# Performance work log

Hardware: AMD Instinct MI355X
Metric: run time of the kernel (lower is better)

## Reference

```python
import jax, jax.numpy as jnp
import numpy as np

T, D, H = 2048, 1024, 16
HS = D // H  # head_size = 64
DFF = 4 * D
LN_EPS = 1e-6


def layernorm(x, scale, bias, eps=LN_EPS):
    mu = jnp.mean(x, axis=-1, keepdims=True)
    var = jnp.mean(jnp.square(x - mu), axis=-1, keepdims=True)
    return (x - mu) * jax.lax.rsqrt(var + eps) * scale + bias


def setup_inputs() -> dict:
    key = jax.random.key(0)
    ks = jax.random.split(key, 12)
    s_in = 1.0 / np.sqrt(D)
    s_ff = 1.0 / np.sqrt(DFF)
    return {
        "x": jax.random.normal(ks[0], (T, D), jnp.float32),
        "Wq": jax.random.normal(ks[1], (H, D, HS), jnp.float32) * s_in,
        "Wk": jax.random.normal(ks[2], (H, D, HS), jnp.float32) * s_in,
        "Wv": jax.random.normal(ks[3], (H, D, HS), jnp.float32) * s_in,
        "Wo": jax.random.normal(ks[4], (D, D), jnp.float32) * s_in,
        "bo": jnp.zeros((D,), jnp.float32),
        "W1": jax.random.normal(ks[5], (D, DFF), jnp.float32) * s_in,
        "b1": jnp.zeros((DFF,), jnp.float32),
        "W2": jax.random.normal(ks[6], (DFF, D), jnp.float32) * s_ff,
        "b2": jnp.zeros((D,), jnp.float32),
        "ln1_scale": jnp.ones((D,), jnp.float32),
        "ln1_bias": jnp.zeros((D,), jnp.float32),
        "ln2_scale": jnp.ones((D,), jnp.float32),
        "ln2_bias": jnp.zeros((D,), jnp.float32),
        "training": 0,
    }


def reference(x, Wq, Wk, Wv, Wo, bo, W1, b1, W2, b2,
              ln1_scale, ln1_bias, ln2_scale, ln2_bias, training):
    # --- pre-LN causal multi-head self-attention ---
    h = layernorm(x, ln1_scale, ln1_bias)
    q = jnp.einsum("td,hdk->htk", h, Wq)  # [H,T,HS]
    k = jnp.einsum("td,hdk->htk", h, Wk)
    v = jnp.einsum("td,hdk->htk", h, Wv)
    scores = jnp.einsum("htk,hsk->hts", q, k) / jnp.sqrt(jnp.float32(HS))
    causal = jnp.tril(jnp.ones((T, T), jnp.float32))
    scores = jnp.where(causal == 0, -jnp.inf, scores)
    wei = jax.nn.softmax(scores, axis=-1)
    av = jnp.einsum("hts,hsk->htk", wei, v)          # [H,T,HS]
    av = av.transpose(1, 0, 2).reshape(T, H * HS)    # concat over heads
    x = x + av @ Wo + bo                              # dropout deterministic -> identity
    # --- pre-LN feed-forward ---
    h2 = layernorm(x, ln2_scale, ln2_bias)
    ff = jax.nn.relu(h2 @ W1 + b1) @ W2 + b2
    x = x + ff
    return x
```

## Files before the change

### kernel.cpp

```cpp
#include <hip/hip_runtime.h>
#include <cstdint>


typedef __bf16 bf16;
typedef __bf16 bf16x4 __attribute__((ext_vector_type(4)));
typedef __bf16 bf16x8 __attribute__((ext_vector_type(8)));
typedef float floatx4 __attribute__((ext_vector_type(4)));

__device__ __forceinline__ void ld_g2l(const bf16* g, bf16* l) {
    __builtin_amdgcn_global_load_lds(
        (const __attribute__((address_space(1))) void*)g,
        (__attribute__((address_space(3))) void*)l, 16, 0, 0);
}

__device__ __forceinline__ void ln_row_body(
    const float* __restrict__ x, const float* __restrict__ sc,
    const float* __restrict__ bi, bf16* __restrict__ out,
    int row, int tid, float* wred)
{
    const float4 v = ((const float4*)(x + (size_t)row * 1024))[tid];
    float s1 = v.x + v.y + v.z + v.w;
    float s2 = v.x * v.x + v.y * v.y + v.z * v.z + v.w * v.w;
#pragma unroll
    for (int mm = 1; mm < 64; mm <<= 1) {
        s1 += __shfl_xor(s1, mm);
        s2 += __shfl_xor(s2, mm);
    }
    const int wave = tid >> 6, lane = tid & 63;
    if (lane == 0) { wred[wave] = s1; wred[4 + wave] = s2; }
    __syncthreads();
    s1 = wred[0] + wred[1] + wred[2] + wred[3];
    s2 = wred[4] + wred[5] + wred[6] + wred[7];
    const float mu = s1 * (1.f / 1024.f);
    const float var = fmaxf(s2 * (1.f / 1024.f) - mu * mu, 0.f);
    const float rr = rsqrtf(var + 1e-6f);
    const float4 scv = ((const float4*)sc)[tid];
    const float4 biv = ((const float4*)bi)[tid];
    bf16x4 ov;
    ov[0] = (bf16)((v.x - mu) * rr * scv.x + biv.x);
    ov[1] = (bf16)((v.y - mu) * rr * scv.y + biv.y);
    ov[2] = (bf16)((v.z - mu) * rr * scv.z + biv.z);
    ov[3] = (bf16)((v.w - mu) * rr * scv.w + biv.w);
    *(bf16x4*)(out + (size_t)row * 1024 + tid * 4) = ov;
}

__global__ __launch_bounds__(256) void prep_kernel(
    const float* __restrict__ Wq, const float* __restrict__ Wk,
    const float* __restrict__ Wv, bf16* __restrict__ Wqkvt,
    const float* __restrict__ Wo, bf16* __restrict__ Wot,
    const float* __restrict__ W1, bf16* __restrict__ W1t,
    const float* __restrict__ W2, bf16* __restrict__ W2t,
    const float* __restrict__ x, const float* __restrict__ ln1s,
    const float* __restrict__ ln1b, bf16* __restrict__ hbuf)
{
    __shared__ float tile[64][65];
    __shared__ float wred[8];
    const int b = blockIdx.x;
    const int tid = threadIdx.x;

    if (b >= 3072) {
        ln_row_body(x, ln1s, ln1b, hbuf, b - 3072, tid, wred);
        return;
    }

    const int tx = tid & 63, ty = tid >> 6;
    const float* src; bf16* dst; int R, C, c0, r0;
    if (b < 768) {
        const int sec = b >> 4, ti = b & 15;
        const int m = sec >> 4, h = sec & 15;
        src = (m == 0 ? Wq : (m == 1 ? Wk : Wv)) + h * 65536;
        dst = Wqkvt + m * 1048576 + h * 65536;
        R = 1024; C = 64; c0 = 0; r0 = ti * 64;
    } else if (b < 1024) {
        const int i = b - 768;
        src = Wo; dst = Wot; R = 1024; C = 1024;
        c0 = (i & 15) * 64; r0 = (i >> 4) * 64;
    } else if (b < 2048) {
        const int i = b - 1024;
        src = W1; dst = W1t; R = 1024; C = 4096;
        c0 = (i & 63) * 64; r0 = (i >> 6) * 64;
    } else {
        const int i = b - 2048;
        src = W2; dst = W2t; R = 4096; C = 1024;
        c0 = (i & 15) * 64; r0 = (i >> 4) * 64;
    }
#pragma unroll
    for (int i = ty; i < 64; i += 4)
        tile[i][tx] = src[(size_t)(r0 + i) * C + c0 + tx];
    __syncthreads();
#pragma unroll
    for (int i = ty; i < 64; i += 4)
        dst[(size_t)(c0 + i) * R + r0 + tx] = (bf16)tile[tx][i];
}

__global__ __launch_bounds__(256) void ln_kernel(
    const float* __restrict__ x, const float* __restrict__ sc,
    const float* __restrict__ bi, bf16* __restrict__ out)
{
    __shared__ float wred[8];
    ln_row_body(x, sc, bi, out, blockIdx.x, threadIdx.x, wred);
}

__global__ __launch_bounds__(256) void reduce4_kernel(
    const bf16* __restrict__ p, const float* __restrict__ bias,
    const float* __restrict__ res, float* __restrict__ out)
{
    const int idx = blockIdx.x * 256 + threadIdx.x;
    const size_t e = (size_t)idx * 8;
    const int c = (int)(e & 1023);
    const bf16x8 a0 = *(const bf16x8*)(p + e);
    const bf16x8 a1 = *(const bf16x8*)(p + 2097152 + e);
    const bf16x8 a2 = *(const bf16x8*)(p + 4194304 + e);
    const bf16x8 a3 = *(const bf16x8*)(p + 6291456 + e);
    const float4 b0 = *(const float4*)(bias + c);
    const float4 b1 = *(const float4*)(bias + c + 4);
    const float4 r0 = *(const float4*)(res + e);
    const float4 r1 = *(const float4*)(res + e + 4);
    float o[8];
#pragma unroll
    for (int i = 0; i < 8; ++i)
        o[i] = ((float)a0[i] + (float)a1[i]) + ((float)a2[i] + (float)a3[i]);
    float4 o0, o1;
    o0.x = o[0] + b0.x + r0.x; o0.y = o[1] + b0.y + r0.y;
    o0.z = o[2] + b0.z + r0.z; o0.w = o[3] + b0.w + r0.w;
    o1.x = o[4] + b1.x + r1.x; o1.y = o[5] + b1.y + r1.y;
    o1.z = o[6] + b1.z + r1.z; o1.w = o[7] + b1.w + r1.w;
    *(float4*)(out + e) = o0;
    *(float4*)(out + e + 4) = o1;
}

template <int MODE, int NG, int MG, int SPLITK>
__global__ __launch_bounds__(512) void gemm128_kernel(
    const bf16* __restrict__ A, const bf16* __restrict__ Bt,
    int N, int K,
    float* __restrict__ outF, bf16* __restrict__ outB,
    const float* __restrict__ bias)
{
    __shared__ __align__(16) bf16 Alds[2][128][64];
    __shared__ __align__(16) bf16 Blds[2][128][64];
    const int tid  = threadIdx.x;
    const int lane = tid & 63;
    const int w    = tid >> 6;
    const int r15  = lane & 15;
    const int quad = lane >> 4;

    const int id    = blockIdx.x + gridDim.x * (blockIdx.y + gridDim.y * blockIdx.z);
    const int xcd   = id & 7;
    const int seq   = id >> 3;
    const int nPerX = gridDim.x / NG;
    const int mPerX = gridDim.y / MG;
    const int nm    = nPerX * mPerX;
    const int z     = seq / nm;
    const int loc   = seq - z * nm;
    const int bn    = ((xcd % NG) * nPerX + (loc % nPerX)) * 128;
    const int bm    = ((xcd / NG) * mPerX + (loc / nPerX)) * 128;

    const int wm = (w >> 2) * 64;
    const int wn = (w & 3) * 32;

    floatx4 acc[4][2];
#pragma unroll
    for (int i = 0; i < 4; ++i)
#pragma unroll
        for (int j = 0; j < 2; ++j) acc[i][j] = (floatx4)(0.f);

    const int KS    = K / SPLITK;
    const int kBase = (SPLITK > 1) ? z * KS : 0;
    const int nIter = KS / 64;

    const int lrow = lane >> 3;
    const int gch  = (lane & 7) ^ lrow;
    const bf16* aptr = A + (size_t)(bm + w * 16 + lrow) * K + kBase + gch * 8;
    const bf16* bptr = Bt + (size_t)(bn + w * 16 + lrow) * K + kBase + gch * 8;

#pragma unroll
    for (int t = 0; t < 2; ++t) {
        ld_g2l(aptr + (size_t)(t * 8) * K, &Alds[0][w * 16 + t * 8][0]);
        ld_g2l(bptr + (size_t)(t * 8) * K, &Blds[0][w * 16 + t * 8][0]);
    }

    for (int it = 0; it < nIter; ++it) {
        const int buf = it & 1;
        __syncthreads();
        if (it + 1 < nIter) {
            const int k2 = (it + 1) * 64;
#pragma unroll
            for (int t = 0; t < 2; ++t) {
                ld_g2l(aptr + (size_t)(t * 8) * K + k2, &Alds[buf ^ 1][w * 16 + t * 8][0]);
                ld_g2l(bptr + (size_t)(t * 8) * K + k2, &Blds[buf ^ 1][w * 16 + t * 8][0]);
            }
        }
#pragma unroll
        for (int kk = 0; kk < 2; ++kk) {
            const int pc = ((kk * 4 + quad) ^ (r15 & 7)) * 8;
            bf16x8 af[4], bfr[2];
#pragma unroll
            for (int i = 0; i < 4; ++i)
                af[i] = *(const bf16x8*)(&Alds[buf][wm + i * 16 + r15][pc]);
#pragma unroll
            for (int j = 0; j < 2; ++j)
                bfr[j] = *(const bf16x8*)(&Blds[buf][wn + j * 16 + r15][pc]);
#pragma unroll
            for (int i = 0; i < 4; ++i)
#pragma unroll
                for (int j = 0; j < 2; ++j)
                    acc[i][j] = __builtin_amdgcn_mfma_f32_16x16x32_bf16(
                        af[i], bfr[j], acc[i][j], 0, 0, 0);
        }
    }

    const int row0 = bm + wm + quad * 4;
    const int col0 = bn + wn + r15;

    if (MODE == 1 && bn >= 2048) {
        bf16* vt = (bf16*)outF;
#pragma unroll
        for (int i = 0; i < 4; ++i) {
            const int row = row0 + i * 16;
#pragma unroll
            for (int j = 0; j < 2; ++j) {
                const int col = col0 + j * 16 - 2048;
                bf16x4 pv;
#pragma unroll
                for (int reg = 0; reg < 4; ++reg) pv[reg] = (bf16)acc[i][j][reg];
                *(bf16x4*)(vt + (size_t)(col >> 6) * 131072
                              + (size_t)(col & 63) * 2048 + row) = pv;
            }
        }
        return;
    }

    bf16* po = (MODE == 3) ? outB + (size_t)z * 2097152 : outB;
#pragma unroll
    for (int i = 0; i < 4; ++i) {
#pragma unroll
        for (int reg = 0; reg < 4; ++reg) {
            const int row = row0 + i * 16 + reg;
#pragma unroll
            for (int j = 0; j < 2; ++j) {
                const int col = col0 + j * 16;
                float v = acc[i][j][reg];
                if (MODE == 0 || MODE == 1) {
                    outB[(size_t)row * N + col] = (bf16)v;
                } else if (MODE == 2) {
                    v += bias[col];
                    outB[(size_t)row * N + col] = (bf16)fmaxf(v, 0.f);
                } else {
                    po[(size_t)row * N + col] = (bf16)v;
                }
            }
        }
    }
}

template <int NG, int MG>
__global__ __launch_bounds__(256) void oproj_kernel(
    const bf16* __restrict__ Opart, const float* __restrict__ Lpart,
    const bf16* __restrict__ Bt,
    float* __restrict__ outF, const float* __restrict__ bias,
    const float* __restrict__ res)
{
    const int N = 1024, K = 1024;
    __shared__ __align__(16) bf16 Alds[2][64][64];
    __shared__ __align__(16) bf16 Blds[2][64][64];
    const int tid  = threadIdx.x;
    const int lane = tid & 63;
    const int w    = tid >> 6;
    const int r15  = lane & 15;
    const int quad = lane >> 4;

    const int id    = blockIdx.x + gridDim.x * blockIdx.y;
    const int xcd   = id & 7;
    const int seq   = id >> 3;
    const int nPerX = gridDim.x / NG;
    const int mPerX = gridDim.y / MG;
    const int loc   = seq % (nPerX * mPerX);
    const int bn    = ((xcd % NG) * nPerX + (loc % nPerX)) * 64;
    const int bm    = ((xcd / NG) * mPerX + (loc / nPerX)) * 64;

    const int wm = (w >> 1) * 32;
    const int wn = (w & 1) * 32;
    const int qt = bm >> 6;
    const bool hasB = (qt > 0);

    floatx4 acc[2][2];
#pragma unroll
    for (int i = 0; i < 2; ++i)
#pragma unroll
        for (int j = 0; j < 2; ++j) acc[i][j] = (floatx4)(0.f);

    const int nIter = K / 64;
    const int lrow = lane >> 3;
    const int gch  = (lane & 7) ^ lrow;
    const bf16* bptr = Bt + (size_t)(bn + w * 16 + lrow) * K + gch * 8;

    const int rit0 = w * 16 + lrow;
    const int rit1 = rit0 + 8;

#pragma unroll
    for (int t = 0; t < 2; ++t)
        ld_g2l(bptr + (size_t)(t * 8) * K, &Blds[0][w * 16 + t * 8][0]);
    {
        const size_t tb = (size_t)qt * 4096;
#pragma unroll
        for (int t = 0; t < 2; ++t) {
            const int rit = t ? rit1 : rit0;
            const size_t off = tb + (size_t)rit * 64 + gch * 8;
            const bf16x8 a = *(const bf16x8*)(Opart + off);
            float la = Lpart[qt * 64 + rit];
            bf16x8 bv; float lb = 0.f;
#pragma unroll
            for (int i = 0; i < 8; ++i) bv[i] = (bf16)0.f;
            if (hasB) {
                bv = *(const bf16x8*)(Opart + 2097152 + off);
                lb = Lpart[32768 + qt * 64 + rit];
            }
            const float inv = 1.f / (la + lb);
            bf16x8 o;
#pragma unroll
            for (int i = 0; i < 8; ++i)
                o[i] = (bf16)(((float)a[i] + (float)bv[i]) * inv);
            *(bf16x8*)(&Alds[0][w * 16 + t * 8 + lrow][(lane & 7) * 8]) = o;
        }
    }

    for (int it = 0; it < nIter; ++it) {
        const int buf = it & 1;
        __syncthreads();
        bf16x8 na[2], nb[2];
        float nla[2], nlb[2];
        const bool pf = (it + 1 < nIter);
        if (pf) {
            const int k2 = (it + 1) * 64;
#pragma unroll
            for (int t = 0; t < 2; ++t)
                ld_g2l(bptr + (size_t)(t * 8) * K + k2, &Blds[buf ^ 1][w * 16 + t * 8][0]);
            const size_t tb = (size_t)((it + 1) * 32 + qt) * 4096;
#pragma unroll
            for (int t = 0; t < 2; ++t) {
                const int rit = t ? rit1 : rit0;
                const size_t off = tb + (size_t)rit * 64 + gch * 8;
                na[t] = *(const bf16x8*)(Opart + off);
                nla[t] = Lpart[((it + 1) * 32 + qt) * 64 + rit];
#pragma unroll
                for (int i = 0; i < 8; ++i) nb[t][i] = (bf16)0.f;
                nlb[t] = 0.f;
                if (hasB) {
                    nb[t] = *(const bf16x8*)(Opart + 2097152 + off);
                    nlb[t] = Lpart[32768 + ((it + 1) * 32 + qt) * 64 + rit];
                }
            }
        }
#pragma unroll
        for (int kk = 0; kk < 2; ++kk) {
            const int pc = ((kk * 4 + quad) ^ (r15 & 7)) * 8;
            bf16x8 af[2], bfr[2];
#pragma unroll
            for (int i = 0; i < 2; ++i)
                af[i] = *(const bf16x8*)(&Alds[buf][wm + i * 16 + r15][pc]);
#pragma unroll
            for (int j = 0; j < 2; ++j)
                bfr[j] = *(const bf16x8*)(&Blds[buf][wn + j * 16 + r15][pc]);
#pragma unroll
            for (int i = 0; i < 2; ++i)
#pragma unroll
                for (int j = 0; j < 2; ++j)
                    acc[i][j] = __builtin_amdgcn_mfma_f32_16x16x32_bf16(
                        af[i], bfr[j], acc[i][j], 0, 0, 0);
        }
        if (pf) {
#pragma unroll
            for (int t = 0; t < 2; ++t) {
                const float inv = 1.f / (nla[t] + nlb[t]);
                bf16x8 o;
#pragma unroll
                for (int i = 0; i < 8; ++i)
                    o[i] = (bf16)(((float)na[t][i] + (float)nb[t][i]) * inv);
                *(bf16x8*)(&Alds[buf ^ 1][w * 16 + t * 8 + lrow][(lane & 7) * 8]) = o;
            }
        }
    }

    const int row0 = bm + wm + quad * 4;
    const int col0 = bn + wn + r15;
#pragma unroll
    for (int i = 0; i < 2; ++i)
#pragma unroll
        for (int reg = 0; reg < 4; ++reg) {
            const int row = row0 + i * 16 + reg;
#pragma unroll
            for (int j = 0; j < 2; ++j) {
                const int col = col0 + j * 16;
                outF[(size_t)row * N + col] =
                    acc[i][j][reg] + bias[col] + res[(size_t)row * N + col];
            }
        }
}

__global__ __launch_bounds__(256) void attn_kernel(
    const bf16* __restrict__ qkv, const bf16* __restrict__ vt,
    bf16* __restrict__ Opart, float* __restrict__ Lpart)
{
    __shared__ __align__(16) bf16 Qs[64][64];
    __shared__ __align__(16) bf16 Ks[2][64][64];
    __shared__ __align__(16) bf16 Vs[2][64][64];
    __shared__ __align__(16) bf16 Ps[4][16][72];

    const int tid  = threadIdx.x;
    const int w    = tid >> 6;
    const int lane = tid & 63;
    const int r15  = lane & 15;
    const int quad = lane >> 4;
    const int rl   = lane >> 3;
    const int gsw  = (lane & 7) ^ (rl & 7);

    const int b    = blockIdx.x;
    const int idp  = b & 255;
    const int seq  = idp >> 3;
    const int h    = (idp & 7) * 2 + (seq & 1);
    const int qp   = seq >> 1;
    const int qt   = ((b >> 8) & 1) ? 31 - qp : qp;
    const int half = b >> 9;
    const int qrow0 = qt * 64;

    const int n0    = (qt + 2) >> 1;
    const int sbBeg = half ? n0 : 0;
    const int sbEnd = half ? qt + 1 : n0;

    if (sbBeg >= sbEnd) return;

    const int tile = half * 512 + h * 32 + qt;
    const size_t obase = (size_t)tile * 4096;

    const bf16* qsec = qkv + h * 64;
    const bf16* ksec = qkv + 1024 + h * 64;
    const bf16* vth  = vt + (size_t)h * 64 * 2048;
    const int s0 = sbBeg * 64;

#pragma unroll
    for (int t = 0; t < 2; ++t) {
        const int r = t * 32 + w * 8 + rl;
        ld_g2l(qsec + (size_t)(qrow0 + r) * 3072 + gsw * 8, &Qs[t * 32 + w * 8][0]);
        ld_g2l(ksec + (size_t)(s0 + r) * 3072 + gsw * 8, &Ks[0][t * 32 + w * 8][0]);
        ld_g2l(vth + (size_t)r * 2048 + s0 + gsw * 8, &Vs[0][t * 32 + w * 8][0]);
    }
    __syncthreads();

    bf16x8 qf[2];
#pragma unroll
    for (int c = 0; c < 2; ++c) {
        const int p = ((c * 4 + quad) ^ (r15 & 7)) * 8;
        qf[c] = *(const bf16x8*)&Qs[w * 16 + r15][p];
    }

    float lacc[4] = {0.f, 0.f, 0.f, 0.f};
    floatx4 O[4];
#pragma unroll
    for (int j = 0; j < 4; ++j) O[j] = (floatx4)(0.f);

    int ns = 0;
#pragma unroll 1
    for (int sb = sbBeg; sb < sbEnd; ++sb, ++ns) {
        const int buf = ns & 1;
        if (sb + 1 < sbEnd) {
            const int s1 = (sb + 1) * 64;
#pragma unroll
            for (int t = 0; t < 2; ++t) {
                const int r = t * 32 + w * 8 + rl;
                ld_g2l(ksec + (size_t)(s1 + r) * 3072 + gsw * 8, &Ks[buf ^ 1][t * 32 + w * 8][0]);
                ld_g2l(vth + (size_t)r * 2048 + s1 + gsw * 8, &Vs[buf ^ 1][t * 32 + w * 8][0]);
            }
        }

        floatx4 S[4];
#pragma unroll
        for (int j = 0; j < 4; ++j) S[j] = (floatx4)(0.f);
        __builtin_amdgcn_s_setprio(1);
#pragma unroll
        for (int c = 0; c < 2; ++c) {
#pragma unroll
            for (int j = 0; j < 4; ++j) {
                const int p = ((c * 4 + quad) ^ (r15 & 7)) * 8;
                const bf16x8 kb = *(const bf16x8*)&Ks[buf][j * 16 + r15][p];
                S[j] = __builtin_amdgcn_mfma_f32_16x16x32_bf16(qf[c], kb, S[j], 0, 0, 0);
            }
        }
        __builtin_amdgcn_s_setprio(0);
        if (sb == qt) {
            const int rowl = w * 16 + quad * 4;
#pragma unroll
            for (int j = 0; j < 4; ++j) {
                const int col = j * 16 + r15;
#pragma unroll
                for (int r = 0; r < 4; ++r) {
                    float p = exp2f(fmaf(S[j][r], 0.18033688f, -28.853901f));
                    if (col > rowl + r) p = 0.f;
                    S[j][r] = p;
                    lacc[r] += p;
                }
            }
        } else {
#pragma unroll
            for (int j = 0; j < 4; ++j)
#pragma unroll
                for (int r = 0; r < 4; ++r) {
                    const float p = exp2f(fmaf(S[j][r], 0.18033688f, -28.853901f));
                    S[j][r] = p;
                    lacc[r] += p;
                }
        }
#pragma unroll
        for (int r = 0; r < 4; ++r)
#pragma unroll
            for (int j = 0; j < 4; ++j)
                Ps[w][quad * 4 + r][j * 16 + r15] = (bf16)S[j][r];
        __builtin_amdgcn_s_setprio(1);
#pragma unroll
        for (int c = 0; c < 2; ++c) {
            const bf16x8 a = *(const bf16x8*)&Ps[w][r15][c * 32 + quad * 8];
#pragma unroll
            for (int j = 0; j < 4; ++j) {
                const int p = ((c * 4 + quad) ^ (r15 & 7)) * 8;
                const bf16x8 vb = *(const bf16x8*)&Vs[buf][j * 16 + r15][p];
                O[j] = __builtin_amdgcn_mfma_f32_16x16x32_bf16(a, vb, O[j], 0, 0, 0);
            }
        }
        __builtin_amdgcn_s_setprio(0);
        __syncthreads();
    }
#pragma unroll
    for (int r = 0; r < 4; ++r) {
#pragma unroll
        for (int d = 1; d < 16; d <<= 1) lacc[r] += __shfl_xor(lacc[r], d);
    }
#pragma unroll
    for (int r = 0; r < 4; ++r) {
        const int row = w * 16 + quad * 4 + r;
#pragma unroll
        for (int j = 0; j < 4; ++j)
            Opart[obase + (size_t)row * 64 + j * 16 + r15] = (bf16)(O[j][r]);
    }
    if (r15 == 0) {
#pragma unroll
        for (int r = 0; r < 4; ++r)
            Lpart[tile * 64 + w * 16 + quad * 4 + r] = lacc[r];
    }
}

extern "C" void kernel_launch(void* const* d_in, const int* in_sizes, int n_in,
                              void* d_out, int out_size, void* d_ws, size_t ws_size,
                              hipStream_t stream)
{
    const float* x    = (const float*)d_in[0];
    const float* Wq   = (const float*)d_in[1];
    const float* Wk   = (const float*)d_in[2];
    const float* Wv   = (const float*)d_in[3];
    const float* Wo   = (const float*)d_in[4];
    const float* bo   = (const float*)d_in[5];
    const float* W1   = (const float*)d_in[6];
    const float* b1   = (const float*)d_in[7];
    const float* W2   = (const float*)d_in[8];
    const float* b2   = (const float*)d_in[9];
    const float* ln1s = (const float*)d_in[10];
    const float* ln1b = (const float*)d_in[11];
    const float* ln2s = (const float*)d_in[12];
    const float* ln2b = (const float*)d_in[13];

    char* ws = (char*)d_ws;
    bf16*  Wqkvt = (bf16*)(ws + 0);
    bf16*  Wot   = (bf16*)(ws + 6291456);
    bf16*  W1t   = (bf16*)(ws + 8388608);
    bf16*  W2t   = (bf16*)(ws + 16777216);
    bf16*  hbuf  = (bf16*)(ws + 25165824);
    bf16*  QKV   = (bf16*)(ws + 29360128);
    bf16*  Vt    = (bf16*)(ws + 41943040);
    float* x1    = (float*)(ws + 50331648);
    bf16*  h2    = (bf16*)(ws + 58720256);
    bf16*  ff1   = (bf16*)(ws + 62914560);
    bf16*  psum  = (bf16*)(ws + 79691776);
    bf16*  Opart = (bf16*)(ws + 79691776);
    float* Lpart = (float*)(ws + 96468992);

    prep_kernel<<<5120, 256, 0, stream>>>(Wq, Wk, Wv, Wqkvt, Wo, Wot,
                                          W1, W1t, W2, W2t,
                                          x, ln1s, ln1b, hbuf);
    gemm128_kernel<1,4,2,1><<<dim3(24, 16), 512, 0, stream>>>(hbuf, Wqkvt, 3072, 1024, (float*)Vt, QKV, nullptr);
    attn_kernel<<<1024, 256, 0, stream>>>(QKV, Vt, Opart, Lpart);
    oproj_kernel<4,2><<<dim3(16, 32), 256, 0, stream>>>(Opart, Lpart, Wot, x1, bo, x);
    ln_kernel<<<2048, 256, 0, stream>>>(x1, ln2s, ln2b, h2);
    gemm128_kernel<2,4,2,1><<<dim3(32, 16), 512, 0, stream>>>(h2, W1t, 4096, 1024, nullptr, ff1, b1);
    gemm128_kernel<3,2,4,4><<<dim3(8, 16, 4), 512, 0, stream>>>(ff1, W2t, 1024, 4096, nullptr, psum, nullptr);
    reduce4_kernel<<<1024, 256, 0, stream>>>(psum, b2, x1, (float*)d_out);
}
```

Before: 246.3 us.

## Move Wo/W1/W2 transposes into attention kernel to overlap with attention

The Wo, W1 and W2 fp32-to-bf16 transpose work moves out of the prep kernel, which now only handles Wqkv and LN1. It runs as extra blocks appended to the attention launch, sharing LDS through a union. The goal is to fill idle CUs during the causally imbalanced attention and shorten the critical path before the QKV GEMM. The risk is that transpose blocks compete with attention blocks for bandwidth and CU slots, and the larger union can cut attention occupancy.

```diff
diff --git a/kernel.cpp b/kernel.cpp
--- a/kernel.cpp
+++ b/kernel.cpp
@@ -47,9 +47,6 @@
 __global__ __launch_bounds__(256) void prep_kernel(
     const float* __restrict__ Wq, const float* __restrict__ Wk,
     const float* __restrict__ Wv, bf16* __restrict__ Wqkvt,
-    const float* __restrict__ Wo, bf16* __restrict__ Wot,
-    const float* __restrict__ W1, bf16* __restrict__ W1t,
-    const float* __restrict__ W2, bf16* __restrict__ W2t,
     const float* __restrict__ x, const float* __restrict__ ln1s,
     const float* __restrict__ ln1b, bf16* __restrict__ hbuf)
 {
@@ -58,39 +55,24 @@
     const int b = blockIdx.x;
     const int tid = threadIdx.x;
 
-    if (b >= 3072) {
-        ln_row_body(x, ln1s, ln1b, hbuf, b - 3072, tid, wred);
+    if (b >= 768) {
+        ln_row_body(x, ln1s, ln1b, hbuf, b - 768, tid, wred);
         return;
     }
 
     const int tx = tid & 63, ty = tid >> 6;
-    const float* src; bf16* dst; int R, C, c0, r0;
-    if (b < 768) {
-        const int sec = b >> 4, ti = b & 15;
-        const int m = sec >> 4, h = sec & 15;
-        src = (m == 0 ? Wq : (m == 1 ? Wk : Wv)) + h * 65536;
-        dst = Wqkvt + m * 1048576 + h * 65536;
-        R = 1024; C = 64; c0 = 0; r0 = ti * 64;
-    } else if (b < 1024) {
-        const int i = b - 768;
-        src = Wo; dst = Wot; R = 1024; C = 1024;
-        c0 = (i & 15) * 64; r0 = (i >> 4) * 64;
-    } else if (b < 2048) {
-        const int i = b - 1024;
-        src = W1; dst = W1t; R = 1024; C = 4096;
-        c0 = (i & 63) * 64; r0 = (i >> 6) * 64;
-    } else {
-        const int i = b - 2048;
-        src = W2; dst = W2t; R = 4096; C = 1024;
-        c0 = (i & 15) * 64; r0 = (i >> 4) * 64;
-    }
+    const int sec = b >> 4, ti = b & 15;
+    const int m = sec >> 4, h = sec & 15;
+    const float* src = (m == 0 ? Wq : (m == 1 ? Wk : Wv)) + h * 65536;
+    bf16* dst = Wqkvt + m * 1048576 + h * 65536;
+    const int r0 = ti * 64;
 #pragma unroll
     for (int i = ty; i < 64; i += 4)
-        tile[i][tx] = src[(size_t)(r0 + i) * C + c0 + tx];
+        tile[i][tx] = src[(size_t)(r0 + i) * 64 + tx];
     __syncthreads();
 #pragma unroll
     for (int i = ty; i < 64; i += 4)
-        dst[(size_t)(c0 + i) * R + r0 + tx] = (bf16)tile[tx][i];
+        dst[(size_t)i * 1024 + r0 + tx] = (bf16)tile[tx][i];
 }
 
 __global__ __launch_bounds__(256) void ln_kernel(
@@ -399,14 +381,50 @@
 
 __global__ __launch_bounds__(256) void attn_kernel(
     const bf16* __restrict__ qkv, const bf16* __restrict__ vt,
-    bf16* __restrict__ Opart, float* __restrict__ Lpart)
-{
-    __shared__ __align__(16) bf16 Qs[64][64];
-    __shared__ __align__(16) bf16 Ks[2][64][64];
-    __shared__ __align__(16) bf16 Vs[2][64][64];
-    __shared__ __align__(16) bf16 Ps[4][16][72];
+    bf16* __restrict__ Opart, float* __restrict__ Lpart,
+    const float* __restrict__ Wo, bf16* __restrict__ Wot,
+    const float* __restrict__ W1, bf16* __restrict__ W1t,
+    const float* __restrict__ W2, bf16* __restrict__ W2t)
+{
+    __shared__ __align__(16) union SM {
+        struct {
+            bf16 Qs[64][64];
+            bf16 Ks[2][64][64];
+            bf16 Vs[2][64][64];
+            bf16 Ps[4][16][72];
+        } a;
+        float tile[64][65];
+    } sm;
 
     const int tid  = threadIdx.x;
+    const int b    = blockIdx.x;
+
+    if (b >= 1024) {
+        const int i = b - 1024;
+        const float* src; bf16* dst; int R, C, c0, r0;
+        if (i < 256) {
+            src = Wo; dst = Wot; R = 1024; C = 1024;
+            c0 = (i & 15) * 64; r0 = (i >> 4) * 64;
+        } else if (i < 1280) {
+            const int j = i - 256;
+            src = W1; dst = W1t; R = 1024; C = 4096;
+            c0 = (j & 63) * 64; r0 = (j >> 6) * 64;
+        } else {
+            const int j = i - 1280;
+            src = W2; dst = W2t; R = 4096; C = 1024;
+            c0 = (j & 15) * 64; r0 = (j >> 4) * 64;
+        }
+        const int tx = tid & 63, ty = tid >> 6;
+#pragma unroll
+        for (int k = ty; k < 64; k += 4)
+            sm.tile[k][tx] = src[(size_t)(r0 + k) * C + c0 + tx];
+        __syncthreads();
+#pragma unroll
+        for (int k = ty; k < 64; k += 4)
+            dst[(size_t)(c0 + k) * R + r0 + tx] = (bf16)sm.tile[tx][k];
+        return;
+    }
+
     const int w    = tid >> 6;
     const int lane = tid & 63;
     const int r15  = lane & 15;
@@ -414,7 +432,6 @@
     const int rl   = lane >> 3;
     const int gsw  = (lane & 7) ^ (rl & 7);
 
-    const int b    = blockIdx.x;
     const int idp  = b & 255;
     const int seq  = idp >> 3;
     const int h    = (idp & 7) * 2 + (seq & 1);
@@ -440,9 +457,9 @@
 #pragma unroll
     for (int t = 0; t < 2; ++t) {
         const int r = t * 32 + w * 8 + rl;
-        ld_g2l(qsec + (size_t)(qrow0 + r) * 3072 + gsw * 8, &Qs[t * 32 + w * 8][0]);
-        ld_g2l(ksec + (size_t)(s0 + r) * 3072 + gsw * 8, &Ks[0][t * 32 + w * 8][0]);
-        ld_g2l(vth + (size_t)r * 2048 + s0 + gsw * 8, &Vs[0][t * 32 + w * 8][0]);
+        ld_g2l(qsec + (size_t)(qrow0 + r) * 3072 + gsw * 8, &sm.a.Qs[t * 32 + w * 8][0]);
+        ld_g2l(ksec + (size_t)(s0 + r) * 3072 + gsw * 8, &sm.a.Ks[0][t * 32 + w * 8][0]);
+        ld_g2l(vth + (size_t)r * 2048 + s0 + gsw * 8, &sm.a.Vs[0][t * 32 + w * 8][0]);
     }
     __syncthreads();
 
@@ -450,7 +467,7 @@
 #pragma unroll
     for (int c = 0; c < 2; ++c) {
         const int p = ((c * 4 + quad) ^ (r15 & 7)) * 8;
-        qf[c] = *(const bf16x8*)&Qs[w * 16 + r15][p];
+        qf[c] = *(const bf16x8*)&sm.a.Qs[w * 16 + r15][p];
     }
 
     float lacc[4] = {0.f, 0.f, 0.f, 0.f};
@@ -467,8 +484,8 @@
 #pragma unroll
             for (int t = 0; t < 2; ++t) {
                 const int r = t * 32 + w * 8 + rl;
-                ld_g2l(ksec + (size_t)(s1 + r) * 3072 + gsw * 8, &Ks[buf ^ 1][t * 32 + w * 8][0]);
-                ld_g2l(vth + (size_t)r * 2048 + s1 + gsw * 8, &Vs[buf ^ 1][t * 32 + w * 8][0]);
+                ld_g2l(ksec + (size_t)(s1 + r) * 3072 + gsw * 8, &sm.a.Ks[buf ^ 1][t * 32 + w * 8][0]);
+                ld_g2l(vth + (size_t)r * 2048 + s1 + gsw * 8, &sm.a.Vs[buf ^ 1][t * 32 + w * 8][0]);
             }
         }
 
@@ -481,7 +498,7 @@
 #pragma unroll
             for (int j = 0; j < 4; ++j) {
                 const int p = ((c * 4 + quad) ^ (r15 & 7)) * 8;
-                const bf16x8 kb = *(const bf16x8*)&Ks[buf][j * 16 + r15][p];
+                const bf16x8 kb = *(const bf16x8*)&sm.a.Ks[buf][j * 16 + r15][p];
                 S[j] = __builtin_amdgcn_mfma_f32_16x16x32_bf16(qf[c], kb, S[j], 0, 0, 0);
             }
         }
@@ -513,15 +530,15 @@
         for (int r = 0; r < 4; ++r)
 #pragma unroll
             for (int j = 0; j < 4; ++j)
-                Ps[w][quad * 4 + r][j * 16 + r15] = (bf16)S[j][r];
+                sm.a.Ps[w][quad * 4 + r][j * 16 + r15] = (bf16)S[j][r];
         __builtin_amdgcn_s_setprio(1);
 #pragma unroll
         for (int c = 0; c < 2; ++c) {
-            const bf16x8 a = *(const bf16x8*)&Ps[w][r15][c * 32 + quad * 8];
+            const bf16x8 a = *(const bf16x8*)&sm.a.Ps[w][r15][c * 32 + quad * 8];
 #pragma unroll
             for (int j = 0; j < 4; ++j) {
                 const int p = ((c * 4 + quad) ^ (r15 & 7)) * 8;
-                const bf16x8 vb = *(const bf16x8*)&Vs[buf][j * 16 + r15][p];
+                const bf16x8 vb = *(const bf16x8*)&sm.a.Vs[buf][j * 16 + r15][p];
                 O[j] = __builtin_amdgcn_mfma_f32_16x16x32_bf16(a, vb, O[j], 0, 0, 0);
             }
         }
@@ -581,11 +598,10 @@
     bf16*  Opart = (bf16*)(ws + 79691776);
     float* Lpart = (float*)(ws + 96468992);
 
-    prep_kernel<<<5120, 256, 0, stream>>>(Wq, Wk, Wv, Wqkvt, Wo, Wot,
-                                          W1, W1t, W2, W2t,
-                                          x, ln1s, ln1b, hbuf);
+    prep_kernel<<<2816, 256, 0, stream>>>(Wq, Wk, Wv, Wqkvt, x, ln1s, ln1b, hbuf);
     gemm128_kernel<1,4,2,1><<<dim3(24, 16), 512, 0, stream>>>(hbuf, Wqkvt, 3072, 1024, (float*)Vt, QKV, nullptr);
-    attn_kernel<<<1024, 256, 0, stream>>>(QKV, Vt, Opart, Lpart);
+    attn_kernel<<<3328, 256, 0, stream>>>(QKV, Vt, Opart, Lpart,
+                                          Wo, Wot, W1, W1t, W2, W2t);
     oproj_kernel<4,2><<<dim3(16, 32), 256, 0, stream>>>(Opart, Lpart, Wot, x1, bo, x);
     ln_kernel<<<2048, 256, 0, stream>>>(x1, ln2s, ln2b, h2);
     gemm128_kernel<2,4,2,1><<<dim3(32, 16), 512, 0, stream>>>(h2, W1t, 4096, 1024, nullptr, ff1, b1);
```

Result: no change. 246.2 us (-0.0%).
